# Kernel optimization log

Hardware: AMD Instinct MI355X
Metric: run time of the kernel (lower is better)

## Reference

```python
import jax, jax.numpy as jnp
import numpy as np

HS = 4096
NIN = 17   # RFSIZE*RFSIZE + ADDINPUT + NBACTIONS = 9 + 4 + 4
NACT = 4


def setup_inputs() -> dict:
    key = jax.random.key(0)
    ks = jax.random.split(key, 10)
    return {
        "inputs": jax.random.normal(ks[0], (1, NIN), jnp.float32),
        "hidden": jax.random.normal(ks[1], (1, HS), jnp.float32) * 0.1,
        "hebb": jnp.zeros((HS, HS), jnp.float32),
        "et": jnp.zeros((HS, HS), jnp.float32),
        "pw": jnp.zeros((HS, HS), jnp.float32),
        # i2h Linear(17 -> hs)
        "i2h_w": jax.random.normal(ks[2], (HS, NIN), jnp.float32) * (1.0 / np.sqrt(NIN)),
        "i2h_b": jax.random.normal(ks[3], (HS,), jnp.float32) * 0.01,
        # plastic recurrent params: 0.01 * rand, eta = 0.01 * ones(1)
        "w": 0.01 * jax.random.uniform(ks[4], (HS, HS), jnp.float32),
        "alpha": 0.01 * jax.random.uniform(ks[5], (HS, HS), jnp.float32),
        "eta": 0.01 * jnp.ones((1,), jnp.float32),
        # output heads
        "h2o_w": jax.random.normal(ks[6], (NACT, HS), jnp.float32) * (1.0 / np.sqrt(HS)),
        "h2o_b": jax.random.normal(ks[7], (NACT,), jnp.float32) * 0.01,
        "h2v_w": jax.random.normal(ks[8], (1, HS), jnp.float32) * (1.0 / np.sqrt(HS)),
        "h2v_b": jax.random.normal(ks[9], (1,), jnp.float32) * 0.01,
    }


def reference(inputs, hidden, hebb, et, pw,
              i2h_w, i2h_b, w, alpha, eta,
              h2o_w, h2o_b, h2v_w, h2v_b):
    # type='plastic', rule='hebb', clp=0, addpw=0
    # hactiv = tanh(i2h(inputs) + hidden @ (w + alpha * hebb))
    pre = inputs @ i2h_w.T + i2h_b + hidden @ (w + alpha * hebb)  # [1, HS]
    hactiv = jnp.tanh(pre)
    activout = hactiv @ h2o_w.T + h2o_b   # [1, NBACTIONS]
    valueout = hactiv @ h2v_w.T + h2v_b   # [1, 1]
    # deltahebb = outer(hidden[0], hactiv[0])  (batch 1, matches torch.bmm(...)[0])
    deltahebb = hidden[0][:, None] * hactiv[0][None, :]  # [HS, HS]
    hebb_new = (1.0 - eta) * hebb + eta * deltahebb       # eta shape (1,) broadcasts
    # hidden <- hactiv; et, pw untouched for this type
    return activout, valueout, hactiv, hebb_new, et, pw
```

## Files before the change

kernel.cpp:

```cpp
#include <hip/hip_runtime.h>
#include <math.h>

#define HS 4096
#define NIN 17
#define ROW_CHUNKS 128
#define ROWS_PER_CHUNK (HS / ROW_CHUNKS)

__global__ __launch_bounds__(256) void matvec_partial_k(
    const float* __restrict__ hidden, const float* __restrict__ w,
    const float* __restrict__ alpha, const float* __restrict__ hebb,
    float* __restrict__ partial) {
  const int j4 = blockIdx.x * blockDim.x + threadIdx.x;
  const int row0 = blockIdx.y * ROWS_PER_CHUNK;
  const size_t base = (size_t)row0 * (HS / 4) + j4;
  const float4* wp = reinterpret_cast<const float4*>(w) + base;
  const float4* ap = reinterpret_cast<const float4*>(alpha) + base;
  const float4* bp = reinterpret_cast<const float4*>(hebb) + base;
  float4 acc = make_float4(0.f, 0.f, 0.f, 0.f);
  for (int r = 0; r < ROWS_PER_CHUNK; ++r) {
    const float h = hidden[row0 + r];
    const float4 wv = wp[(size_t)r * (HS / 4)];
    const float4 av = ap[(size_t)r * (HS / 4)];
    const float4 bv = bp[(size_t)r * (HS / 4)];
    acc.x = fmaf(h, fmaf(av.x, bv.x, wv.x), acc.x);
    acc.y = fmaf(h, fmaf(av.y, bv.y, wv.y), acc.y);
    acc.z = fmaf(h, fmaf(av.z, bv.z, wv.z), acc.z);
    acc.w = fmaf(h, fmaf(av.w, bv.w, wv.w), acc.w);
  }
  reinterpret_cast<float4*>(partial)[(size_t)blockIdx.y * (HS / 4) + j4] = acc;
}

__global__ __launch_bounds__(256) void finalize_k(
    const float* __restrict__ partial, const float* __restrict__ inputs,
    const float* __restrict__ i2h_w, const float* __restrict__ i2h_b,
    float* __restrict__ out_hactiv) {
  const int j = blockIdx.x * blockDim.x + threadIdx.x;
  float s = i2h_b[j];
#pragma unroll
  for (int k = 0; k < NIN; ++k) s = fmaf(inputs[k], i2h_w[j * NIN + k], s);
  float r = 0.f;
  for (int c = 0; c < ROW_CHUNKS; ++c) r += partial[c * HS + j];
  out_hactiv[j] = tanhf(s + r);
}

__global__ __launch_bounds__(256) void heads_k(
    const float* __restrict__ hactiv, const float* __restrict__ h2o_w,
    const float* __restrict__ h2o_b, const float* __restrict__ h2v_w,
    const float* __restrict__ h2v_b, float* __restrict__ out) {
  const int r = blockIdx.x;
  const float* wrow = (r < 4) ? (h2o_w + (size_t)r * HS) : h2v_w;
  float s = 0.f;
  for (int j = threadIdx.x; j < HS; j += 256) s = fmaf(hactiv[j], wrow[j], s);
  __shared__ float red[256];
  red[threadIdx.x] = s;
  __syncthreads();
  for (int off = 128; off > 0; off >>= 1) {
    if (threadIdx.x < off) red[threadIdx.x] += red[threadIdx.x + off];
    __syncthreads();
  }
  if (threadIdx.x == 0) {
    const float b = (r < 4) ? h2o_b[r] : h2v_b[0];
    out[r] = red[0] + b;
  }
}

__global__ __launch_bounds__(256) void hebb_update_k(
    const float* __restrict__ hebb, const float* __restrict__ hidden,
    const float* __restrict__ hactiv, const float* __restrict__ eta,
    float* __restrict__ out) {
  const int t = blockIdx.x * blockDim.x + threadIdx.x;
  const int i = t >> 12;
  const int j = t & (HS - 1);
  const float e = eta[0];
  out[t] = (1.f - e) * hebb[t] + e * hidden[i] * hactiv[j];
}

__global__ __launch_bounds__(256) void copy_k(
    const float* __restrict__ src, float* __restrict__ dst) {
  const int t = blockIdx.x * blockDim.x + threadIdx.x;
  dst[t] = src[t];
}

extern "C" void kernel_launch(void* const* d_in, const int* in_sizes, int n_in,
                              void* d_out, int out_size, void* d_ws, size_t ws_size,
                              hipStream_t stream) {
  const float* inputs = (const float*)d_in[0];
  const float* hidden = (const float*)d_in[1];
  const float* hebb   = (const float*)d_in[2];
  const float* et     = (const float*)d_in[3];
  const float* pw     = (const float*)d_in[4];
  const float* i2h_w  = (const float*)d_in[5];
  const float* i2h_b  = (const float*)d_in[6];
  const float* w      = (const float*)d_in[7];
  const float* alpha  = (const float*)d_in[8];
  const float* eta    = (const float*)d_in[9];
  const float* h2o_w  = (const float*)d_in[10];
  const float* h2o_b  = (const float*)d_in[11];
  const float* h2v_w  = (const float*)d_in[12];
  const float* h2v_b  = (const float*)d_in[13];

  float* out = (float*)d_out;
  const size_t NSQ = (size_t)HS * HS;
  float* out_heads  = out;
  float* out_hactiv = out + 5;
  float* out_hebb   = out + 5 + HS;
  float* out_et     = out_hebb + NSQ;
  float* out_pw     = out_et + NSQ;

  const size_t need = (size_t)ROW_CHUNKS * HS * sizeof(float);
  float* partial = (ws_size >= need) ? (float*)d_ws
                                     : (out_hebb + 3 );

  dim3 mv_grid(HS / 4 / 256, ROW_CHUNKS);
  hipLaunchKernelGGL(matvec_partial_k, mv_grid, dim3(256), 0, stream,
                     hidden, w, alpha, hebb, partial);
  hipLaunchKernelGGL(finalize_k, dim3(HS / 256), dim3(256), 0, stream,
                     partial, inputs, i2h_w, i2h_b, out_hactiv);
  hipLaunchKernelGGL(heads_k, dim3(5), dim3(256), 0, stream,
                     out_hactiv, h2o_w, h2o_b, h2v_w, h2v_b, out_heads);
  hipLaunchKernelGGL(hebb_update_k, dim3((unsigned)(NSQ / 256)), dim3(256), 0, stream,
                     hebb, hidden, out_hactiv, eta, out_hebb);
  hipLaunchKernelGGL(copy_k, dim3((unsigned)(NSQ / 256)), dim3(256), 0, stream,
                     et, out_et);
  hipLaunchKernelGGL(copy_k, dim3((unsigned)(NSQ / 256)), dim3(256), 0, stream,
                     pw, out_pw);
}
```

Measured before the change: 503.4 us.

## Fuse hebb update and copies into one grid-stride kernel, widen matvec split

The hebb update and the two et/pw copy kernels are merged into a single persistent grid-stride kernel with 2048 blocks, which removes two launches and the per-element grid overhead. The matvec row split goes from 128 to 512 chunks with the inner loop unrolled, giving more blocks for latency hiding. The cost is a larger partial buffer that finalize must reduce, now 512 entries per column, and that buffer may not fit in the workspace. The elementwise kernel still uses scalar accesses.

Result: faster. 488.5 us (-3.0%).

```diff
diff --git a/kernel.cpp b/kernel.cpp
--- a/kernel.cpp
+++ b/kernel.cpp
@@ -3,7 +3,7 @@
 
 #define HS 4096
 #define NIN 17
-#define ROW_CHUNKS 128
+#define ROW_CHUNKS 512
 #define ROWS_PER_CHUNK (HS / ROW_CHUNKS)
 
 __global__ __launch_bounds__(256) void matvec_partial_k(
@@ -17,6 +17,7 @@
   const float4* ap = reinterpret_cast<const float4*>(alpha) + base;
   const float4* bp = reinterpret_cast<const float4*>(hebb) + base;
   float4 acc = make_float4(0.f, 0.f, 0.f, 0.f);
+#pragma unroll
   for (int r = 0; r < ROWS_PER_CHUNK; ++r) {
     const float h = hidden[row0 + r];
     const float4 wv = wp[(size_t)r * (HS / 4)];
@@ -39,7 +40,7 @@
 #pragma unroll
   for (int k = 0; k < NIN; ++k) s = fmaf(inputs[k], i2h_w[j * NIN + k], s);
   float r = 0.f;
-  for (int c = 0; c < ROW_CHUNKS; ++c) r += partial[c * HS + j];
+  for (int c = 0; c < ROW_CHUNKS; ++c) r += partial[(size_t)c * HS + j];
   out_hactiv[j] = tanhf(s + r);
 }
 
@@ -64,21 +65,24 @@
   }
 }
 
-__global__ __launch_bounds__(256) void hebb_update_k(
+__global__ __launch_bounds__(256) void elementwise_k(
     const float* __restrict__ hebb, const float* __restrict__ hidden,
     const float* __restrict__ hactiv, const float* __restrict__ eta,
-    float* __restrict__ out) {
-  const int t = blockIdx.x * blockDim.x + threadIdx.x;
-  const int i = t >> 12;
-  const int j = t & (HS - 1);
+    const float* __restrict__ et, const float* __restrict__ pw,
+    float* __restrict__ out_hebb, float* __restrict__ out_et,
+    float* __restrict__ out_pw) {
+  const unsigned NSQ = (unsigned)HS * HS;
+  const unsigned stride = gridDim.x * blockDim.x;
+  const unsigned tid = blockIdx.x * blockDim.x + threadIdx.x;
   const float e = eta[0];
-  out[t] = (1.f - e) * hebb[t] + e * hidden[i] * hactiv[j];
-}
-
-__global__ __launch_bounds__(256) void copy_k(
-    const float* __restrict__ src, float* __restrict__ dst) {
-  const int t = blockIdx.x * blockDim.x + threadIdx.x;
-  dst[t] = src[t];
+  const float one_m_e = 1.f - e;
+  for (unsigned t = tid; t < NSQ; t += stride) {
+    const float hi = hidden[t >> 12];
+    const float ha = hactiv[t & (HS - 1)];
+    out_hebb[t] = fmaf(one_m_e, hebb[t], e * hi * ha);
+  }
+  for (unsigned t = tid; t < NSQ; t += stride) out_et[t] = et[t];
+  for (unsigned t = tid; t < NSQ; t += stride) out_pw[t] = pw[t];
 }
 
 extern "C" void kernel_launch(void* const* d_in, const int* in_sizes, int n_in,
@@ -111,17 +115,13 @@
   float* partial = (ws_size >= need) ? (float*)d_ws
                                      : (out_hebb + 3 );
 
-  dim3 mv_grid(HS / 4 / 256, ROW_CHUNKS);
-  hipLaunchKernelGGL(matvec_partial_k, mv_grid, dim3(256), 0, stream,
-                     hidden, w, alpha, hebb, partial);
+  hipLaunchKernelGGL(matvec_partial_k, dim3(HS / 4 / 256, ROW_CHUNKS), dim3(256),
+                     0, stream, hidden, w, alpha, hebb, partial);
   hipLaunchKernelGGL(finalize_k, dim3(HS / 256), dim3(256), 0, stream,
                      partial, inputs, i2h_w, i2h_b, out_hactiv);
   hipLaunchKernelGGL(heads_k, dim3(5), dim3(256), 0, stream,
                      out_hactiv, h2o_w, h2o_b, h2v_w, h2v_b, out_heads);
-  hipLaunchKernelGGL(hebb_update_k, dim3((unsigned)(NSQ / 256)), dim3(256), 0, stream,
-                     hebb, hidden, out_hactiv, eta, out_hebb);
-  hipLaunchKernelGGL(copy_k, dim3((unsigned)(NSQ / 256)), dim3(256), 0, stream,
-                     et, out_et);
-  hipLaunchKernelGGL(copy_k, dim3((unsigned)(NSQ / 256)), dim3(256), 0, stream,
-                     pw, out_pw);
+  hipLaunchKernelGGL(elementwise_k, dim3(2048), dim3(256), 0, stream,
+                     hebb, hidden, out_hactiv, eta, et, pw,
+                     out_hebb, out_et, out_pw);
 }
```
